# Performance work log

Measured on AMD Instinct MI355X. Metric: run time of the kernel, lower is better.

## Reference

```python
import jax, jax.numpy as jnp
from jax import lax
import numpy as np

N, C, H, W = 8, 128, 96, 96
G, K = 8, 3                      # groups, kernel_size
GC = C // G                      # group channels = 16
STRIDE, PAD, DIL = 1, 1, 1
OFFSET_SCALE = 1.0
OM_DIM = int(np.ceil(G * K * K * 3 / 8) * 8)   # 216 (== G*K*K*3, no padding)
GN_EPS = 1e-5


def setup_inputs() -> dict:
    key = jax.random.key(0)
    ks = jax.random.split(key, 7)
    inp = {
        "input": jax.random.normal(ks[0], (N, C, H, W), dtype=jnp.float32),
        # depthwise conv (Conv2d groups=C): OIHW with I=1
        "dw_w": jax.random.normal(ks[1], (C, 1, K, K), dtype=jnp.float32) * 0.1,
        "dw_b": jax.random.normal(ks[2], (C,), dtype=jnp.float32) * 0.05,
        # GroupNorm(num_groups=1) affine params
        "gn_w": jnp.ones((C,), dtype=jnp.float32),
        "gn_b": jnp.zeros((C,), dtype=jnp.float32),
        # offset_mask Linear (module zero-inits; use small random for a meaningful test)
        "om_w": jax.random.normal(ks[3], (OM_DIM, C), dtype=jnp.float32) * 0.02,
        "om_b": jax.random.normal(ks[4], (OM_DIM,), dtype=jnp.float32) * 0.02,
    }
    return inp


def _dcnv4_forward(x, dw_w, dw_b, gn_w, gn_b, om_w, om_b):
    # x: (N, C, H, W)
    # ---- offset/mask branch: depthwise conv -> GroupNorm(1) -> GELU -> Linear
    x1 = lax.conv_general_dilated(
        x, dw_w, window_strides=(1, 1), padding=[(1, 1), (1, 1)],
        feature_group_count=C, dimension_numbers=("NCHW", "OIHW", "NCHW"))
    x1 = x1 + dw_b[None, :, None, None]
    mu = jnp.mean(x1, axis=(1, 2, 3), keepdims=True)
    var = jnp.var(x1, axis=(1, 2, 3), keepdims=True)
    x1 = (x1 - mu) * lax.rsqrt(var + GN_EPS)
    x1 = x1 * gn_w[None, :, None, None] + gn_b[None, :, None, None]
    x1 = jax.nn.gelu(x1, approximate=False)
    x1 = jnp.transpose(x1, (0, 2, 3, 1))                     # (N,H,W,C)
    om = jnp.einsum("nhwc,oc->nhwo", x1, om_w) + om_b        # (N,H,W,216)

    K2 = K * K
    om = om[..., : G * K2 * 3].reshape(N, H, W, G, K2 * 3)
    offs = om[..., : 2 * K2].reshape(N, H, W, G, K2, 2)      # (dx, dy) per point
    mask = om[..., 2 * K2:]                                  # (N,H,W,G,K2), no softmax in DCNv4

    # ---- sampling locations (pixel coords in the unpadded input, zeros outside)
    ky, kx = jnp.meshgrid(jnp.arange(K), jnp.arange(K), indexing="ij")
    base_y = ((ky - (K - 1) / 2.0) * DIL).reshape(-1).astype(jnp.float32)  # (K2,)
    base_x = ((kx - (K - 1) / 2.0) * DIL).reshape(-1).astype(jnp.float32)
    ctr_y = jnp.arange(H, dtype=jnp.float32) * STRIDE - PAD + DIL * (K - 1) / 2.0
    ctr_x = jnp.arange(W, dtype=jnp.float32) * STRIDE - PAD + DIL * (K - 1) / 2.0
    loc_y = ctr_y[None, :, None, None, None] + (base_y + offs[..., 1]) * OFFSET_SCALE
    loc_x = ctr_x[None, None, :, None, None] + (base_x + offs[..., 0]) * OFFSET_SCALE

    # ---- grouped bilinear gather
    xv = jnp.transpose(x, (0, 2, 3, 1)).reshape(N, H, W, G, GC)   # values, channels-last
    y0 = jnp.floor(loc_y)
    x0 = jnp.floor(loc_x)
    ly = loc_y - y0
    lx = loc_x - x0
    y0i = y0.astype(jnp.int32)
    x0i = x0.astype(jnp.int32)
    n_idx = jnp.arange(N)[:, None, None, None, None]
    g_idx = jnp.arange(G)[None, None, None, :, None]

    def gather(yi, xi):
        valid = (yi >= 0) & (yi < H) & (xi >= 0) & (xi < W)
        yc = jnp.clip(yi, 0, H - 1)
        xc = jnp.clip(xi, 0, W - 1)
        v = xv[n_idx, yc, xc, g_idx]                 # (N,H,W,G,K2,GC)
        return v * valid[..., None].astype(xv.dtype)

    samp = (gather(y0i,     x0i)     * ((1 - ly) * (1 - lx))[..., None]
          + gather(y0i,     x0i + 1) * ((1 - ly) * lx)[..., None]
          + gather(y0i + 1, x0i)     * (ly * (1 - lx))[..., None]
          + gather(y0i + 1, x0i + 1) * (ly * lx)[..., None])

    out = jnp.sum(samp * mask[..., None], axis=4)    # (N,H,W,G,GC)
    out = out.reshape(N, H, W, C)
    return jnp.transpose(out, (0, 3, 1, 2))          # (N,C,H,W)


def reference(input, dw_w, dw_b, gn_w, gn_b, om_w, om_b):
    return _dcnv4_forward(input, dw_w, dw_b, gn_w, gn_b, om_w, om_b)
```

## Files before the change

### kernel.cpp

```cpp
#include <hip/hip_runtime.h>
#include <hip/hip_bf16.h>

#define N_   8
#define C_   128
#define H_   96
#define W_   96
#define G_   8
#define GC_  16
#define HW_  (H_ * W_)
#define CHW_ (C_ * HW_)
#define OM_  216
#define OMP_ 224
#define OMROWS2_ 112
#define EPS_ 1e-5f
#define BLKS_PER_N_ 192
#define PW_  100
#define PPLANE_ (PW_ * PW_ * GC_)

typedef short bf16x8 __attribute__((ext_vector_type(8)));
typedef float f32x4 __attribute__((ext_vector_type(4)));

#if __has_builtin(__builtin_amdgcn_fdot2_f32_bf16)
#define HAVE_DOT2_ 1
typedef __bf16 bf16x2 __attribute__((ext_vector_type(2)));
static __device__ __forceinline__ bf16x2 u2bf2(unsigned int u) {
  union { unsigned int i; bf16x2 v; } c;
  c.i = u;
  return c.v;
}
#else
#define HAVE_DOT2_ 0
#endif

static __device__ __forceinline__ unsigned short f2bf(float f) {
  unsigned int u = __float_as_uint(f);
  unsigned int r = (u + 0x7fffu + ((u >> 16) & 1u)) >> 16;
  return (unsigned short)r;
}
static __device__ __forceinline__ unsigned int pk_bf2(float lo, float hi) {
  __hip_bfloat162 h = __float22bfloat162_rn(make_float2(lo, hi));
  union { __hip_bfloat162 h; unsigned int u; } c;
  c.h = h;
  return c.u;
}
static __device__ __forceinline__ float lo_bf(unsigned int u) {
  return __uint_as_float(u << 16);
}
static __device__ __forceinline__ float hi_bf(unsigned int u) {
  return __uint_as_float(u & 0xffff0000u);
}

static __device__ __forceinline__ float fast_gelu(float z) {
  float s = z * 0.70710678118654752f;
  float as = fabsf(s);
  float t = __builtin_amdgcn_rcpf(fmaf(0.3275911f, as, 1.0f));
  float e = __expf(-as * as);
  float inner = fmaf(fmaf(fmaf(fmaf(1.061405429f, t, -1.453152027f), t,
                               1.421413741f), t, -0.284496736f), t, 0.254829592f);
  float y = fmaf(-inner * t, e, 1.0f);
  float erf_s = copysignf(y, s);
  float hz = 0.5f * z;
  return fmaf(hz, erf_s, hz);
}

template <bool SAFE>
static __device__ __forceinline__ void loadrow5t(float dst[2][5],
                                                 const float* __restrict__ xp0,
                                                 const float* __restrict__ xp1,
                                                 int hh, int w0) {
  bool vy = SAFE ? true : ((hh >= 0) & (hh < H_));
#pragma unroll
  for (int j = 0; j < 5; ++j) {
    int ww = w0 - 1 + j;
    bool v = vy & (ww >= 0) & (ww < W_);
    dst[0][j] = v ? xp0[hh * W_ + ww] : 0.0f;
    dst[1][j] = v ? xp1[hh * W_ + ww] : 0.0f;
  }
}

template <bool SAFE>
static __device__ __forceinline__ void conv_tile(const float* __restrict__ xp0,
                                                 const float* __restrict__ xp1,
                                                 const float wk[2][9],
                                                 const float bias[2],
                                                 int h0, int w0, int ty,
                                                 unsigned int* __restrict__ lds_a,
                                                 unsigned int* __restrict__ lds_c,
                                                 float& s, float& q) {
  float rr[3][2][5];
  loadrow5t<SAFE>(rr[0], xp0, xp1, h0 - 1, w0);
  loadrow5t<SAFE>(rr[1], xp0, xp1, h0,     w0);

#pragma unroll
  for (int r = 0; r < 4; ++r) {
    const int sA = r % 3;
    const int sB = (r + 1) % 3;
    const int sC = (r + 2) % 3;
    loadrow5t<SAFE>(rr[sC], xp0, xp1, h0 + r + 1, w0);

#pragma unroll
    for (int j = 0; j < 3; ++j) {
      float acc0 = bias[0], acc1 = bias[1];
#pragma unroll
      for (int dx = 0; dx < 3; ++dx) {
        acc0 = fmaf(rr[sA][0][j + dx], wk[0][0 + dx], acc0);
        acc1 = fmaf(rr[sA][1][j + dx], wk[1][0 + dx], acc1);
        acc0 = fmaf(rr[sB][0][j + dx], wk[0][3 + dx], acc0);
        acc1 = fmaf(rr[sB][1][j + dx], wk[1][3 + dx], acc1);
        acc0 = fmaf(rr[sC][0][j + dx], wk[0][6 + dx], acc0);
        acc1 = fmaf(rr[sC][1][j + dx], wk[1][6 + dx], acc1);
      }
      float cen0 = rr[sB][0][j + 1];
      float cen1 = rr[sB][1][j + 1];
      s += acc0 + acc1;
      q = fmaf(acc0, acc0, q);
      q = fmaf(acc1, acc1, q);
      int pxl = r * 96 + w0 + j;
      lds_a[pxl * 9 + ty] = pk_bf2(acc0, acc1);
      lds_c[pxl * 9 + ty] = pk_bf2(cen0, cen1);
    }
  }
}

__global__ __launch_bounds__(256) void k_front(const float* __restrict__ x,
                                               const float* __restrict__ dw_w,
                                               const float* __restrict__ dw_b,
                                               unsigned short* __restrict__ xgb,
                                               unsigned short* __restrict__ x1b,
                                               float2* __restrict__ partials,
                                               const float* __restrict__ om_w,
                                               const float* __restrict__ om_b,
                                               unsigned short* __restrict__ A,
                                               float* __restrict__ biasp) {
  int fb = blockIdx.x;
  int tid = threadIdx.x;

  if (fb >= N_ * BLKS_PER_N_) {
    int pb2 = fb - N_ * BLKS_PER_N_;
    if (pb2 < 112) {
      int idx = pb2 * 256 + tid;
      int o = idx >> 7;
      int cix = idx & 127;
      int g = o / 28;
      int k = o - g * 28;
      float v = (k < 27) ? om_w[(g * 27 + k) * C_ + cix] : 0.0f;
      A[idx] = f2bf(v);
      if (cix == 0) biasp[o] = (k < 27) ? om_b[g * 27 + k] : 0.0f;
    } else {
      int gid = (pb2 - 112) * 256 + tid;
      const int NBORD = 64 * 784;
      for (int id = gid; id < NBORD; id += 80 * 256) {
        int plane = id / 784;
        int r = id - plane * 784;
        int row, col;
        if (r < 400) {
          int qq = r / 100;
          row = (qq < 2) ? qq : qq + 96;
          col = r - qq * 100;
        } else {
          int r2 = r - 400;
          int qq = r2 >> 2;
          int c4 = r2 & 3;
          row = 2 + qq;
          col = (c4 < 2) ? c4 : c4 + 96;
        }
        uint4* dst = (uint4*)(xgb + (size_t)plane * PPLANE_ + (row * PW_ + col) * GC_);
        uint4 z = {0, 0, 0, 0};
        dst[0] = z;
        dst[1] = z;
      }
    }
    return;
  }

  __shared__ unsigned int lds_c[384 * 9];
  __shared__ unsigned int lds_a[384 * 9];
  __shared__ float ls[4], lq[4];

  int tx = tid & 31;
  int ty = tid >> 5;
  int n   = fb / BLKS_PER_N_;
  int rem = fb - n * BLKS_PER_N_;
  int g   = rem / 24;
  int hb  = rem - g * 24;
  int h0 = hb * 4;
  int w0 = tx * 3;

  const int c0 = g * 16 + 2 * ty;
  float wk[2][9];
  const float* wp = dw_w + c0 * 9;
#pragma unroll
  for (int j = 0; j < 9; ++j) {
    wk[0][j] = wp[j];
    wk[1][j] = wp[9 + j];
  }
  float bias[2] = {dw_b[c0], dw_b[c0 + 1]};

  const float* xp0 = x + ((size_t)(n * C_ + c0)) * HW_;
  const float* xp1 = xp0 + HW_;

  float s = 0.0f, q = 0.0f;

  if (hb > 0 && hb < 23) {
    conv_tile<true>(xp0, xp1, wk, bias, h0, w0, ty, lds_a, lds_c, s, q);
  } else {
    conv_tile<false>(xp0, xp1, wk, bias, h0, w0, ty, lds_a, lds_c, s, q);
  }
  __syncthreads();

  for (int i = tid; i < 384; i += 256) {
    int row = i / 96;
    int col = i - row * 96;
    unsigned int wc[8], wa[8];
#pragma unroll
    for (int k = 0; k < 8; ++k) {
      wc[k] = lds_c[i * 9 + k];
      wa[k] = lds_a[i * 9 + k];
    }
    unsigned int* xg = (unsigned int*)xgb + (size_t)(n * G_ + g) * (PPLANE_ / 2)
                       + ((h0 + row + 2) * PW_ + (col + 2)) * 8;
    uint4 c01 = {wc[0], wc[1], wc[2], wc[3]};
    uint4 c23 = {wc[4], wc[5], wc[6], wc[7]};
    *(uint4*)xg = c01;
    *(uint4*)(xg + 4) = c23;
    int p = (h0 + row) * W_ + col;
    unsigned int* xb = (unsigned int*)x1b + ((size_t)n * HW_ + p) * 64 + g * 8;
    uint4 a01 = {wa[0], wa[1], wa[2], wa[3]};
    uint4 a23 = {wa[4], wa[5], wa[6], wa[7]};
    *(uint4*)xb = a01;
    *(uint4*)(xb + 4) = a23;
  }

#pragma unroll
  for (int o = 32; o > 0; o >>= 1) {
    s += __shfl_down(s, o);
    q += __shfl_down(q, o);
  }
  int lane = tid & 63;
  int wv = tid >> 6;
  if (lane == 0) { ls[wv] = s; lq[wv] = q; }
  __syncthreads();
  if (tid == 0) {
    partials[fb] = make_float2(ls[0] + ls[1] + ls[2] + ls[3],
                               lq[0] + lq[1] + lq[2] + lq[3]);
  }
}

static __device__ __forceinline__ void pref_af(bf16x8 (&af)[4],
                                               const unsigned short* __restrict__ A,
                                               int ot, int l16, int quad) {
  const unsigned short* Ap = A + (ot * 16 + l16) * C_ + quad * 8;
#pragma unroll
  for (int kk = 0; kk < 4; ++kk) af[kk] = *(const bf16x8*)(Ap + kk * 32);
}

__global__ __launch_bounds__(256) void k_gemm_mfma(const unsigned short* __restrict__ Bt,
                                                   const unsigned short* __restrict__ A,
                                                   const float* __restrict__ biasp,
                                                   const float2* __restrict__ partials,
                                                   const float* __restrict__ gn_w,
                                                   const float* __restrict__ gn_b,
                                                   unsigned int* __restrict__ om2) {
  __shared__ unsigned short Bl[32 * 136];
  __shared__ alignas(16) float s_bias[OMP_];
  __shared__ float ls[4], lq[4];
  int tid = threadIdx.x;
  int pb = blockIdx.x;
  int n = blockIdx.y;
  int p0 = pb * 32;

  const unsigned short* src = Bt + ((size_t)n * HW_ + p0) * C_;
  int col = tid & 15;
  int row0 = tid >> 4;
  uint4 raw0 = *(const uint4*)(src + row0 * C_ + col * 8);
  uint4 raw1 = *(const uint4*)(src + (16 + row0) * C_ + col * 8);
  int cbase = col * 8;
  float gw8[8], gb8[8];
#pragma unroll
  for (int j = 0; j < 8; ++j) {
    gw8[j] = gn_w[cbase + j];
    gb8[j] = gn_b[cbase + j];
  }
  if (tid < OMP_ / 4) {
    ((float4*)s_bias)[tid] = ((const float4*)biasp)[tid];
  }

  {
    float s = 0.0f, q = 0.0f;
    if (tid < BLKS_PER_N_) {
      float2 v = partials[n * BLKS_PER_N_ + tid];
      s = v.x;
      q = v.y;
    }
#pragma unroll
    for (int o = 32; o > 0; o >>= 1) {
      s += __shfl_down(s, o);
      q += __shfl_down(q, o);
    }
    int lane = tid & 63;
    int wv = tid >> 6;
    if (lane == 0) { ls[wv] = s; lq[wv] = q; }
  }
  __syncthreads();

  float sum = ls[0] + ls[1] + ls[2] + ls[3];
  float ssq = lq[0] + lq[1] + lq[2] + lq[3];
  const float inv = 1.0f / (float)CHW_;
  float mean = sum * inv;
  float var = ssq * inv - mean * mean;
  float rstd = rsqrtf(var + EPS_);
  float a8[8], b8[8];
#pragma unroll
  for (int j = 0; j < 8; ++j) {
    a8[j] = rstd * gw8[j];
    b8[j] = gb8[j] - mean * rstd * gw8[j];
  }

  {
    uint4 raws[2] = {raw0, raw1};
#pragma unroll
    for (int i = 0; i < 2; ++i) {
      int row = row0 + i * 16;
      unsigned int d[4] = {raws[i].x, raws[i].y, raws[i].z, raws[i].w};
      unsigned int od[4];
#pragma unroll
      for (int t = 0; t < 4; ++t) {
        float v0 = lo_bf(d[t]);
        float v1 = hi_bf(d[t]);
        float z0 = fmaf(v0, a8[2 * t], b8[2 * t]);
        float z1 = fmaf(v1, a8[2 * t + 1], b8[2 * t + 1]);
        od[t] = pk_bf2(fast_gelu(z0), fast_gelu(z1));
      }
      uint4 packed = {od[0], od[1], od[2], od[3]};
      *(uint4*)(&Bl[row * 136 + col * 8]) = packed;
    }
  }
  __syncthreads();

  int wave = tid >> 6;
  int lane = tid & 63;
  int quad = lane >> 4;
  int l16 = lane & 15;
  int pixhalf = wave & 1;
  int othalf = wave >> 1;
  int prow = pixhalf * 16 + l16;

  bf16x8 bfrag[4];
#pragma unroll
  for (int kk = 0; kk < 4; ++kk)
    bfrag[kk] = *(const bf16x8*)(&Bl[prow * 136 + kk * 32 + quad * 8]);

  int p = p0 + prow;
  int base = othalf * 7;

#define COMP_(AF, OT)                                                          \
  {                                                                            \
    f32x4 acc = {0.f, 0.f, 0.f, 0.f};                                          \
    _Pragma("unroll")                                                          \
    for (int kk = 0; kk < 4; ++kk)                                             \
      acc = __builtin_amdgcn_mfma_f32_16x16x32_bf16(AF[kk], bfrag[kk], acc,    \
                                                    0, 0, 0);                  \
    int o0 = (OT) * 16 + quad * 4;                                             \
    float4 bv = *(const float4*)(&s_bias[o0]);                                 \
    unsigned int pk0 = pk_bf2(acc[0] + bv.x, acc[1] + bv.y);                   \
    unsigned int pk1 = pk_bf2(acc[2] + bv.z, acc[3] + bv.w);                   \
    unsigned int* Cp = om2 + ((size_t)n * OMROWS2_ + (o0 >> 1)) * HW_ + p;     \
    Cp[0] = pk0;                                                               \
    Cp[HW_] = pk1;                                                             \
  }

  bf16x8 af0[4], af1[4];
  pref_af(af0, A, base + 0, l16, quad);
  pref_af(af1, A, base + 1, l16, quad);
  COMP_(af0, base + 0);
  pref_af(af0, A, base + 2, l16, quad);
  COMP_(af1, base + 1);
  pref_af(af1, A, base + 3, l16, quad);
  COMP_(af0, base + 2);
  pref_af(af0, A, base + 4, l16, quad);
  COMP_(af1, base + 3);
  pref_af(af1, A, base + 5, l16, quad);
  COMP_(af0, base + 4);
  pref_af(af0, A, base + 6, l16, quad);
  COMP_(af1, base + 5);
  COMP_(af0, base + 6);
#undef COMP_
}

__global__ __launch_bounds__(256) void k_sample(const unsigned short* __restrict__ xgb,
                                                const unsigned int* __restrict__ om2,
                                                float* __restrict__ out) {
  __shared__ int4 s_wa[9 * 64];

  int tid = threadIdx.x;
  int ord = blockIdx.x;
  int n = ord & 7;
  int t2 = ord >> 3;
  int g = t2 & 7;
  int pb = t2 >> 3;
  int p0 = pb * 64;

  int hb0 = p0 / W_;
  int wb0 = p0 - hb0 * W_;

  const unsigned int* omb = om2 + ((size_t)n * OMROWS2_ + g * 14) * HW_ + p0;
  for (int j = tid; j < 576; j += 256) {
    int pt = j >> 6;
    int px = j & 63;
    int wsum = wb0 + px;
    int carry = wsum >= W_;
    int h = hb0 + carry;
    int w = wsum - (carry ? W_ : 0);
    unsigned int od = omb[pt * HW_ + px];
    float offx = lo_bf(od);
    float offy = hi_bf(od);
    unsigned int md = omb[(9 + (pt >> 1)) * HW_ + px];
    float m = (pt & 1) ? hi_bf(md) : lo_bf(md);
    float locy = (float)(h + pt / 3 - 1) + offy;
    float locx = (float)(w + pt % 3 - 1) + offx;
    float y0f = floorf(locy);
    float x0f = floorf(locx);
    float ly = locy - y0f;
    float lx = locx - x0f;
    int y0 = (int)y0f;
    int x0 = (int)x0f;
    y0 = min(max(y0, -2), 96);
    x0 = min(max(x0, -2), 96);
    float t0 = (1.0f - ly) * m;
    float t1 = ly * m;
    float u0 = 1.0f - lx;
    int4 wa;
    wa.x = (int)pk_bf2(t0 * u0, t1 * u0);
    wa.y = (int)pk_bf2(t0 * lx, t1 * lx);
    wa.z = ((y0 + 2) * PW_ + (x0 + 2)) * (GC_ * 2);
    wa.w = wa.z + PW_ * GC_ * 2;
    s_wa[j] = wa;
  }
  __syncthreads();

  int px_l = tid >> 2;
  int sub = tid & 3;
  int rowhalf = sub >> 1;
  int chunk = sub & 1;
  int p = p0 + px_l;
  const char* xs = (const char*)(xgb + (size_t)(n * G_ + g) * PPLANE_) + sub * 16;

  float acc[8] = {0, 0, 0, 0, 0, 0, 0, 0};

#if HAVE_DOT2_
#define DOT9_(WA, R0, R1)                                                      \
  {                                                                            \
    unsigned int aw = (unsigned int)(rowhalf ? (WA).y : (WA).x);               \
    bf16x2 a2 = u2bf2(aw);                                                     \
    unsigned int d0[4] = {(R0).x, (R0).y, (R0).z, (R0).w};                     \
    unsigned int d1[4] = {(R1).x, (R1).y, (R1).z, (R1).w};                     \
    _Pragma("unroll")                                                          \
    for (int t = 0; t < 4; ++t) {                                              \
      unsigned int blo = __builtin_amdgcn_perm(d1[t], d0[t], 0x05040100u);     \
      unsigned int bhi = __builtin_amdgcn_perm(d1[t], d0[t], 0x07060302u);     \
      acc[2 * t]     = __builtin_amdgcn_fdot2_f32_bf16(a2, u2bf2(blo),         \
                                                       acc[2 * t], false);     \
      acc[2 * t + 1] = __builtin_amdgcn_fdot2_f32_bf16(a2, u2bf2(bhi),         \
                                                       acc[2 * t + 1], false); \
    }                                                                          \
  }
#else
#define DOT9_(WA, R0, R1)                                                      \
  {                                                                            \
    unsigned int aw = (unsigned int)(rowhalf ? (WA).y : (WA).x);               \
    float w0 = lo_bf(aw);                                                      \
    float w1 = hi_bf(aw);                                                      \
    unsigned int d0[4] = {(R0).x, (R0).y, (R0).z, (R0).w};                     \
    unsigned int d1[4] = {(R1).x, (R1).y, (R1).z, (R1).w};                     \
    _Pragma("unroll")                                                          \
    for (int t = 0; t < 4; ++t) {                                              \
      acc[2 * t]     = fmaf(w0, lo_bf(d0[t]), acc[2 * t]);                     \
      acc[2 * t + 1] = fmaf(w0, hi_bf(d0[t]), acc[2 * t + 1]);                 \
      acc[2 * t]     = fmaf(w1, lo_bf(d1[t]), acc[2 * t]);                     \
      acc[2 * t + 1] = fmaf(w1, hi_bf(d1[t]), acc[2 * t + 1]);                 \
    }                                                                          \
  }
#endif

#pragma unroll
  for (int grp = 0; grp < 3; ++grp) {
    int4 waA = s_wa[(grp * 3 + 0) * 64 + px_l];
    int4 waB = s_wa[(grp * 3 + 1) * 64 + px_l];
    int4 waC = s_wa[(grp * 3 + 2) * 64 + px_l];
    uint4 a0 = *(const uint4*)(xs + waA.z);
    uint4 a1 = *(const uint4*)(xs + waA.w);
    uint4 b0 = *(const uint4*)(xs + waB.z);
    uint4 b1 = *(const uint4*)(xs + waB.w);
    uint4 c0 = *(const uint4*)(xs + waC.z);
    uint4 c1 = *(const uint4*)(xs + waC.w);
    DOT9_(waA, a0, a1);
    DOT9_(waB, b0, b1);
    DOT9_(waC, c0, c1);
  }
#undef DOT9_

#pragma unroll
  for (int i = 0; i < 8; ++i) acc[i] += __shfl_xor(acc[i], 2);

  int ch = chunk * 8 + rowhalf * 4;
  float* op = out + ((size_t)(n * C_ + g * GC_ + ch)) * HW_ + p;
#pragma unroll
  for (int r = 0; r < 4; ++r) op[r * HW_] = acc[rowhalf * 4 + r];
}

extern "C" void kernel_launch(void* const* d_in, const int* in_sizes, int n_in,
                              void* d_out, int out_size, void* d_ws, size_t ws_size,
                              hipStream_t stream) {
  const float* x    = (const float*)d_in[0];
  const float* dw_w = (const float*)d_in[1];
  const float* dw_b = (const float*)d_in[2];
  const float* gn_w = (const float*)d_in[3];
  const float* gn_b = (const float*)d_in[4];
  const float* om_w = (const float*)d_in[5];
  const float* om_b = (const float*)d_in[6];
  float* out = (float*)d_out;

  unsigned short* xgb = (unsigned short*)d_ws;
  unsigned short* x1b = xgb + (size_t)64 * PPLANE_;
  unsigned int* om2 = (unsigned int*)(x1b + (size_t)N_ * CHW_);
  float2* partials = (float2*)(om2 + (size_t)N_ * OMROWS2_ * HW_);
  unsigned short* Abf = (unsigned short*)(partials + N_ * BLKS_PER_N_);
  float* biasp = (float*)(Abf + OMP_ * C_);

  k_front<<<N_ * BLKS_PER_N_ + 192, 256, 0, stream>>>(
      x, dw_w, dw_b, xgb, x1b, partials, om_w, om_b, Abf, biasp);
  k_gemm_mfma<<<dim3(HW_ / 32, N_), 256, 0, stream>>>(
      x1b, Abf, biasp, partials, gn_w, gn_b, om2);
  k_sample<<<9216, 256, 0, stream>>>(xgb, om2, out);
}
```

Measured before the change: 178.9 us.

## Fuse offset/mask GEMM into sampling kernel, split GroupNorm+GELU into own pass

The offset/mask projection GEMM is moved into the sampling kernel. Each sampling block computes its group's 32 padded output rows with MFMA for 64 pixels and keeps the results in LDS, so the om2 intermediate no longer makes a global round-trip. GroupNorm and GELU now run as a separate in-place pass over x1b. The trade-off is that the GEMM B-fragments (128 channels per pixel) are reloaded by each of the 8 group blocks, and the padding grows from 28 to 32 rows per group. A scheduling barrier is also added in the sampling inner loop.

```diff
diff --git a/kernel.cpp b/kernel.cpp
--- a/kernel.cpp
+++ b/kernel.cpp
@@ -9,13 +9,11 @@
 #define GC_  16
 #define HW_  (H_ * W_)
 #define CHW_ (C_ * HW_)
-#define OM_  216
-#define OMP_ 224
-#define OMROWS2_ 112
 #define EPS_ 1e-5f
 #define BLKS_PER_N_ 192
 #define PW_  100
 #define PPLANE_ (PW_ * PW_ * GC_)
+#define OMP2_ 256
 
 typedef short bf16x8 __attribute__((ext_vector_type(8)));
 typedef float f32x4 __attribute__((ext_vector_type(4)));
@@ -130,26 +128,26 @@
                                                float2* __restrict__ partials,
                                                const float* __restrict__ om_w,
                                                const float* __restrict__ om_b,
-                                               unsigned short* __restrict__ A,
-                                               float* __restrict__ biasp) {
+                                               unsigned short* __restrict__ A2,
+                                               float* __restrict__ biasp2) {
   int fb = blockIdx.x;
   int tid = threadIdx.x;
 
   if (fb >= N_ * BLKS_PER_N_) {
     int pb2 = fb - N_ * BLKS_PER_N_;
-    if (pb2 < 112) {
+    if (pb2 < 128) {
       int idx = pb2 * 256 + tid;
       int o = idx >> 7;
       int cix = idx & 127;
-      int g = o / 28;
-      int k = o - g * 28;
+      int g = o >> 5;
+      int k = o & 31;
       float v = (k < 27) ? om_w[(g * 27 + k) * C_ + cix] : 0.0f;
-      A[idx] = f2bf(v);
-      if (cix == 0) biasp[o] = (k < 27) ? om_b[g * 27 + k] : 0.0f;
+      A2[idx] = f2bf(v);
+      if (cix == 0) biasp2[o] = (k < 27) ? om_b[g * 27 + k] : 0.0f;
     } else {
-      int gid = (pb2 - 112) * 256 + tid;
+      int gid = (pb2 - 128) * 256 + tid;
       const int NBORD = 64 * 784;
-      for (int id = gid; id < NBORD; id += 80 * 256) {
+      for (int id = gid; id < NBORD; id += 64 * 256) {
         int plane = id / 784;
         int r = id - plane * 784;
         int row, col;
@@ -246,44 +244,14 @@
   }
 }
 
-static __device__ __forceinline__ void pref_af(bf16x8 (&af)[4],
-                                               const unsigned short* __restrict__ A,
-                                               int ot, int l16, int quad) {
-  const unsigned short* Ap = A + (ot * 16 + l16) * C_ + quad * 8;
-#pragma unroll
-  for (int kk = 0; kk < 4; ++kk) af[kk] = *(const bf16x8*)(Ap + kk * 32);
-}
-
-__global__ __launch_bounds__(256) void k_gemm_mfma(const unsigned short* __restrict__ Bt,
-                                                   const unsigned short* __restrict__ A,
-                                                   const float* __restrict__ biasp,
-                                                   const float2* __restrict__ partials,
-                                                   const float* __restrict__ gn_w,
-                                                   const float* __restrict__ gn_b,
-                                                   unsigned int* __restrict__ om2) {
-  __shared__ unsigned short Bl[32 * 136];
-  __shared__ alignas(16) float s_bias[OMP_];
+__global__ __launch_bounds__(256) void k_gelu(unsigned int* __restrict__ x1b,
+                                              const float2* __restrict__ partials,
+                                              const float* __restrict__ gn_w,
+                                              const float* __restrict__ gn_b) {
   __shared__ float ls[4], lq[4];
   int tid = threadIdx.x;
   int pb = blockIdx.x;
   int n = blockIdx.y;
-  int p0 = pb * 32;
-
-  const unsigned short* src = Bt + ((size_t)n * HW_ + p0) * C_;
-  int col = tid & 15;
-  int row0 = tid >> 4;
-  uint4 raw0 = *(const uint4*)(src + row0 * C_ + col * 8);
-  uint4 raw1 = *(const uint4*)(src + (16 + row0) * C_ + col * 8);
-  int cbase = col * 8;
-  float gw8[8], gb8[8];
-#pragma unroll
-  for (int j = 0; j < 8; ++j) {
-    gw8[j] = gn_w[cbase + j];
-    gb8[j] = gn_b[cbase + j];
-  }
-  if (tid < OMP_ / 4) {
-    ((float4*)s_bias)[tid] = ((const float4*)biasp)[tid];
-  }
 
   {
     float s = 0.0f, q = 0.0f;
@@ -309,87 +277,41 @@
   float mean = sum * inv;
   float var = ssq * inv - mean * mean;
   float rstd = rsqrtf(var + EPS_);
+  int ch0 = (tid * 8) & 127;
   float a8[8], b8[8];
 #pragma unroll
   for (int j = 0; j < 8; ++j) {
-    a8[j] = rstd * gw8[j];
-    b8[j] = gb8[j] - mean * rstd * gw8[j];
-  }
-
-  {
-    uint4 raws[2] = {raw0, raw1};
-#pragma unroll
-    for (int i = 0; i < 2; ++i) {
-      int row = row0 + i * 16;
-      unsigned int d[4] = {raws[i].x, raws[i].y, raws[i].z, raws[i].w};
-      unsigned int od[4];
-#pragma unroll
-      for (int t = 0; t < 4; ++t) {
-        float v0 = lo_bf(d[t]);
-        float v1 = hi_bf(d[t]);
-        float z0 = fmaf(v0, a8[2 * t], b8[2 * t]);
-        float z1 = fmaf(v1, a8[2 * t + 1], b8[2 * t + 1]);
-        od[t] = pk_bf2(fast_gelu(z0), fast_gelu(z1));
-      }
-      uint4 packed = {od[0], od[1], od[2], od[3]};
-      *(uint4*)(&Bl[row * 136 + col * 8]) = packed;
-    }
-  }
-  __syncthreads();
-
-  int wave = tid >> 6;
-  int lane = tid & 63;
-  int quad = lane >> 4;
-  int l16 = lane & 15;
-  int pixhalf = wave & 1;
-  int othalf = wave >> 1;
-  int prow = pixhalf * 16 + l16;
-
-  bf16x8 bfrag[4];
-#pragma unroll
-  for (int kk = 0; kk < 4; ++kk)
-    bfrag[kk] = *(const bf16x8*)(&Bl[prow * 136 + kk * 32 + quad * 8]);
-
-  int p = p0 + prow;
-  int base = othalf * 7;
-
-#define COMP_(AF, OT)                                                          \
-  {                                                                            \
-    f32x4 acc = {0.f, 0.f, 0.f, 0.f};                                          \
-    _Pragma("unroll")                                                          \
-    for (int kk = 0; kk < 4; ++kk)                                             \
-      acc = __builtin_amdgcn_mfma_f32_16x16x32_bf16(AF[kk], bfrag[kk], acc,    \
-                                                    0, 0, 0);                  \
-    int o0 = (OT) * 16 + quad * 4;                                             \
-    float4 bv = *(const float4*)(&s_bias[o0]);                                 \
-    unsigned int pk0 = pk_bf2(acc[0] + bv.x, acc[1] + bv.y);                   \
-    unsigned int pk1 = pk_bf2(acc[2] + bv.z, acc[3] + bv.w);                   \
-    unsigned int* Cp = om2 + ((size_t)n * OMROWS2_ + (o0 >> 1)) * HW_ + p;     \
-    Cp[0] = pk0;                                                               \
-    Cp[HW_] = pk1;                                                             \
-  }
-
-  bf16x8 af0[4], af1[4];
-  pref_af(af0, A, base + 0, l16, quad);
-  pref_af(af1, A, base + 1, l16, quad);
-  COMP_(af0, base + 0);
-  pref_af(af0, A, base + 2, l16, quad);
-  COMP_(af1, base + 1);
-  pref_af(af1, A, base + 3, l16, quad);
-  COMP_(af0, base + 2);
-  pref_af(af0, A, base + 4, l16, quad);
-  COMP_(af1, base + 3);
-  pref_af(af1, A, base + 5, l16, quad);
-  COMP_(af0, base + 4);
-  pref_af(af0, A, base + 6, l16, quad);
-  COMP_(af1, base + 5);
-  COMP_(af0, base + 6);
-#undef COMP_
-}
-
-__global__ __launch_bounds__(256) void k_sample(const unsigned short* __restrict__ xgb,
-                                                const unsigned int* __restrict__ om2,
-                                                float* __restrict__ out) {
+    float gw = gn_w[ch0 + j];
+    float gb = gn_b[ch0 + j];
+    a8[j] = rstd * gw;
+    b8[j] = gb - mean * rstd * gw;
+  }
+
+  uint4* bp = (uint4*)x1b + (size_t)(n * HW_ + pb * 64) * 16;
+#pragma unroll
+  for (int jj = 0; jj < 4; ++jj) {
+    uint4 raw = bp[tid + jj * 256];
+    unsigned int d[4] = {raw.x, raw.y, raw.z, raw.w};
+    unsigned int od[4];
+#pragma unroll
+    for (int t = 0; t < 4; ++t) {
+      float v0 = lo_bf(d[t]);
+      float v1 = hi_bf(d[t]);
+      float z0 = fmaf(v0, a8[2 * t], b8[2 * t]);
+      float z1 = fmaf(v1, a8[2 * t + 1], b8[2 * t + 1]);
+      od[t] = pk_bf2(fast_gelu(z0), fast_gelu(z1));
+    }
+    uint4 packed = {od[0], od[1], od[2], od[3]};
+    bp[tid + jj * 256] = packed;
+  }
+}
+
+__global__ __launch_bounds__(256) void k_mfma_sample(const unsigned short* __restrict__ x1g,
+                                                     const unsigned short* __restrict__ A2,
+                                                     const float* __restrict__ biasp2,
+                                                     const unsigned short* __restrict__ xgb,
+                                                     float* __restrict__ out) {
+  __shared__ unsigned int om_lds[16 * 66];
   __shared__ int4 s_wa[9 * 64];
 
   int tid = threadIdx.x;
@@ -400,21 +322,52 @@
   int pb = t2 >> 3;
   int p0 = pb * 64;
 
+  int wave = tid >> 6;
+  int lane = tid & 63;
+  int quad = lane >> 4;
+  int l16 = lane & 15;
+
+  const unsigned short* bsrc =
+      x1g + ((size_t)(n * HW_ + p0 + wave * 16 + l16)) * C_ + quad * 8;
+  bf16x8 bfrag[4];
+#pragma unroll
+  for (int kk = 0; kk < 4; ++kk)
+    bfrag[kk] = *(const bf16x8*)(bsrc + kk * 32);
+
+  int px = wave * 16 + l16;
+#pragma unroll
+  for (int ot2 = 0; ot2 < 2; ++ot2) {
+    const unsigned short* asrc = A2 + (size_t)(g * 32 + ot2 * 16 + l16) * C_ + quad * 8;
+    bf16x8 af[4];
+#pragma unroll
+    for (int kk = 0; kk < 4; ++kk)
+      af[kk] = *(const bf16x8*)(asrc + kk * 32);
+    f32x4 acc = {0.f, 0.f, 0.f, 0.f};
+#pragma unroll
+    for (int kk = 0; kk < 4; ++kk)
+      acc = __builtin_amdgcn_mfma_f32_16x16x32_bf16(af[kk], bfrag[kk], acc, 0, 0, 0);
+    int o0 = ot2 * 16 + quad * 4;
+    float4 bv = *(const float4*)(biasp2 + g * 32 + o0);
+    int r2 = o0 >> 1;
+    om_lds[r2 * 66 + px] = pk_bf2(acc[0] + bv.x, acc[1] + bv.y);
+    om_lds[(r2 + 1) * 66 + px] = pk_bf2(acc[2] + bv.z, acc[3] + bv.w);
+  }
+  __syncthreads();
+
   int hb0 = p0 / W_;
   int wb0 = p0 - hb0 * W_;
 
-  const unsigned int* omb = om2 + ((size_t)n * OMROWS2_ + g * 14) * HW_ + p0;
   for (int j = tid; j < 576; j += 256) {
     int pt = j >> 6;
-    int px = j & 63;
-    int wsum = wb0 + px;
+    int pxj = j & 63;
+    int wsum = wb0 + pxj;
     int carry = wsum >= W_;
     int h = hb0 + carry;
     int w = wsum - (carry ? W_ : 0);
-    unsigned int od = omb[pt * HW_ + px];
+    unsigned int od = om_lds[pt * 66 + pxj];
+    unsigned int md = om_lds[(9 + (pt >> 1)) * 66 + pxj];
     float offx = lo_bf(od);
     float offy = hi_bf(od);
-    unsigned int md = omb[(9 + (pt >> 1)) * HW_ + px];
     float m = (pt & 1) ? hi_bf(md) : lo_bf(md);
     float locy = (float)(h + pt / 3 - 1) + offy;
     float locx = (float)(w + pt % 3 - 1) + offx;
@@ -493,6 +446,7 @@
     uint4 b1 = *(const uint4*)(xs + waB.w);
     uint4 c0 = *(const uint4*)(xs + waC.z);
     uint4 c1 = *(const uint4*)(xs + waC.w);
+    __builtin_amdgcn_sched_barrier(0);
     DOT9_(waA, a0, a1);
     DOT9_(waB, b0, b1);
     DOT9_(waC, c0, c1);
@@ -522,14 +476,13 @@
 
   unsigned short* xgb = (unsigned short*)d_ws;
   unsigned short* x1b = xgb + (size_t)64 * PPLANE_;
-  unsigned int* om2 = (unsigned int*)(x1b + (size_t)N_ * CHW_);
-  float2* partials = (float2*)(om2 + (size_t)N_ * OMROWS2_ * HW_);
-  unsigned short* Abf = (unsigned short*)(partials + N_ * BLKS_PER_N_);
-  float* biasp = (float*)(Abf + OMP_ * C_);
+  float2* partials = (float2*)(x1b + (size_t)N_ * CHW_);
+  unsigned short* A2 = (unsigned short*)(partials + N_ * BLKS_PER_N_);
+  float* biasp2 = (float*)(A2 + (size_t)OMP2_ * C_);
 
   k_front<<<N_ * BLKS_PER_N_ + 192, 256, 0, stream>>>(
-      x, dw_w, dw_b, xgb, x1b, partials, om_w, om_b, Abf, biasp);
-  k_gemm_mfma<<<dim3(HW_ / 32, N_), 256, 0, stream>>>(
-      x1b, Abf, biasp, partials, gn_w, gn_b, om2);
-  k_sample<<<9216, 256, 0, stream>>>(xgb, om2, out);
-}
+      x, dw_w, dw_b, xgb, x1b, partials, om_w, om_b, A2, biasp2);
+  k_gelu<<<dim3(HW_ / 64, N_), 256, 0, stream>>>(
+      (unsigned int*)x1b, partials, gn_w, gn_b);
+  k_mfma_sample<<<9216, 256, 0, stream>>>(x1b, A2, biasp2, xgb, out);
+}
```

Result: slower. 194.5 us (+8.7%).
